# Kernel optimization log

Hardware: AMD Instinct MI355X
Metric: run time of the kernel (lower is better)

The kernel has to match this reference:

```python
import jax, jax.numpy as jnp
import numpy as np

EPS = 1e-6

def rms_norm(x, w):
    xf = x.astype(jnp.float32)
    xf = xf * jax.lax.rsqrt(jnp.mean(jnp.square(xf), axis=-1, keepdims=True) + EPS)
    return xf.astype(x.dtype) * w

def rotate_pairs(x):
    x = x.reshape(*x.shape[:-1], -1, 2)
    x1, x2 = x[..., 0], x[..., 1]
    return jnp.stack((-x2, x1), axis=-1).reshape(*x.shape[:-2], -1)

def apply_rope_axis(x, coords, inv_freq):
    # x: [B, H, T, axis_width]; coords: [T]; inv_freq: [axis_dim]
    angles = coords[:, None].astype(jnp.float32) * inv_freq[None, :]  # [T, axis_dim]
    cos = jnp.repeat(jnp.cos(angles), 2, axis=-1).astype(x.dtype)  # [T, axis_width]
    sin = jnp.repeat(jnp.sin(angles), 2, axis=-1).astype(x.dtype)
    return x * cos[None, None] + rotate_pairs(x) * sin[None, None]

def modulate(x, shift, scale):
    return x * (1.0 + scale[:, None, :]) + shift[:, None, :]

def setup_inputs() -> dict:
    key = jax.random.key(0)
    ks = jax.random.split(key, 16)
    B, T, D = 2, 2048, 1024
    HD = 64            # head_dim
    HID = 4096         # swiglu hidden (dim * mlp_ratio)
    CD = 1024          # cond_dim
    s = lambda n: 1.0 / np.sqrt(n)
    return {
        "x": jax.random.normal(ks[0], (B, T, D), jnp.float32),
        "cond": jax.random.normal(ks[1], (B, CD), jnp.float32),
        "norm1_w": jnp.ones((D,), jnp.float32),
        "qkv_w": jax.random.normal(ks[2], (3 * D, D), jnp.float32) * s(D),
        "q_norm_w": jnp.ones((HD,), jnp.float32),
        "k_norm_w": jnp.ones((HD,), jnp.float32),
        "proj_w": jax.random.normal(ks[3], (D, D), jnp.float32) * s(D),
        "proj_b": jnp.zeros((D,), jnp.float32),
        "norm2_w": jnp.ones((D,), jnp.float32),
        "fc1_w": jax.random.normal(ks[4], (2 * HID, D), jnp.float32) * s(D),
        "fc1_b": jnp.zeros((2 * HID,), jnp.float32),
        "fc2_w": jax.random.normal(ks[5], (D, HID), jnp.float32) * s(HID),
        "fc2_b": jnp.zeros((D,), jnp.float32),
        "ada_w": jax.random.normal(ks[6], (6 * D, CD), jnp.float32) * 0.02,
        "ada_b": jnp.zeros((6 * D,), jnp.float32),
        "height": 64,
        "width": 32,
    }

def reference(x, cond, norm1_w, qkv_w, q_norm_w, k_norm_w, proj_w, proj_b,
              norm2_w, fc1_w, fc1_b, fc2_w, fc2_b, ada_w, ada_b, height, width):
    B, T, D = x.shape
    HD = q_norm_w.shape[0]
    NH = D // HD
    scale = HD ** -0.5
    axis_dim = HD // 4
    axis_w = axis_dim * 2
    inv_freq = 1.0 / (10000.0 ** (jnp.arange(axis_dim, dtype=jnp.float32) / axis_dim))

    # AdaLN-Zero conditioning
    ada = jax.nn.silu(cond) @ ada_w.T + ada_b  # [B, 6D]
    sh_a, sc_a, g_a, sh_m, sc_m, g_m = jnp.split(ada, 6, axis=-1)

    # --- attention branch ---
    residual = x
    h = modulate(rms_norm(x, norm1_w), sh_a, sc_a)
    qkv = (h @ qkv_w.T).reshape(B, T, 3, NH, HD)
    q, k, v = qkv[:, :, 0], qkv[:, :, 1], qkv[:, :, 2]  # [B, T, NH, HD]
    q = rms_norm(q, q_norm_w)
    k = rms_norm(k, k_norm_w)
    q = q.transpose(0, 2, 1, 3)  # [B, NH, T, HD]
    k = k.transpose(0, 2, 1, 3)
    v = v.transpose(0, 2, 1, 3)

    # 2D RoPE: y coords on first axis_w dims, x coords on next axis_w dims
    yy, xx = jnp.meshgrid(jnp.arange(height), jnp.arange(width), indexing="ij")
    yy, xx = yy.reshape(-1), xx.reshape(-1)  # [T]
    q = jnp.concatenate([
        apply_rope_axis(q[..., :axis_w], yy, inv_freq),
        apply_rope_axis(q[..., axis_w:2 * axis_w], xx, inv_freq),
        q[..., 2 * axis_w:]], axis=-1)
    k = jnp.concatenate([
        apply_rope_axis(k[..., :axis_w], yy, inv_freq),
        apply_rope_axis(k[..., axis_w:2 * axis_w], xx, inv_freq),
        k[..., 2 * axis_w:]], axis=-1)

    attn = jax.nn.softmax(jnp.einsum("bhqd,bhkd->bhqk", q, k) * scale, axis=-1)
    h = jnp.einsum("bhqk,bhkd->bhqd", attn, v).transpose(0, 2, 1, 3).reshape(B, T, D)
    h = h @ proj_w.T + proj_b
    x = residual + g_a[:, None, :] * h

    # --- SwiGLU MLP branch ---
    residual = x
    h = modulate(rms_norm(x, norm2_w), sh_m, sc_m)
    value, gate = jnp.split(h @ fc1_w.T + fc1_b, 2, axis=-1)
    h = (value * jax.nn.silu(gate)) @ fc2_w.T + fc2_b
    return residual + g_m[:, None, :] * h
```

## Files before the change

### kernel.cpp

```cpp
#include <hip/hip_runtime.h>
#include <hip/hip_bf16.h>

#define B_   2
#define T_   2048
#define D_   1024
#define NH_  16
#define HD_  64
#define HID_ 4096
#define CD_  1024
#define SIX_D (6*D_)

typedef __bf16 bf16x8 __attribute__((ext_vector_type(8)));
typedef float  f32x4  __attribute__((ext_vector_type(4)));
typedef float  f32x16 __attribute__((ext_vector_type(16)));

__device__ __forceinline__ unsigned short f2bf(float f){
  union { float f; unsigned u; } v; v.f = f;
  unsigned r = v.u + 0x7FFFu + ((v.u >> 16) & 1u);
  return (unsigned short)(r >> 16);
}
__device__ __forceinline__ float bf2f(unsigned short u){
  union { unsigned x; float f; } v; v.x = ((unsigned)u) << 16; return v.f;
}

__device__ __forceinline__ void gl_lds16(const void* g, void* l){
  __builtin_amdgcn_global_load_lds(
      (__attribute__((address_space(1))) void*)const_cast<void*>(g),
      (__attribute__((address_space(3))) void*)l, 16, 0, 0);
}

__global__ void k_conv_all(const float* __restrict__ s0, const float* __restrict__ s1,
                           const float* __restrict__ s2, const float* __restrict__ s3,
                           unsigned short* __restrict__ d0, unsigned short* __restrict__ d1,
                           unsigned short* __restrict__ d2, unsigned short* __restrict__ d3){
  int bid = blockIdx.x;
  const float* s; unsigned short* d; int base;
  if (bid < 3072)      { s = s0; d = d0; base = bid; }
  else if (bid < 4096) { s = s1; d = d1; base = bid - 3072; }
  else if (bid < 12288){ s = s2; d = d2; base = bid - 4096; }
  else                 { s = s3; d = d3; base = bid - 12288; }
  int i = base*256 + threadIdx.x;
  float4 v = reinterpret_cast<const float4*>(s)[i];
  ushort4 o;
  o.x = f2bf(v.x); o.y = f2bf(v.y); o.z = f2bf(v.z); o.w = f2bf(v.w);
  reinterpret_cast<ushort4*>(d)[i] = o;
}

__global__ void k_ada(const float* __restrict__ cond, const float* __restrict__ ada_w,
                      const float* __restrict__ ada_b, float* __restrict__ ada){
  __shared__ float sc[CD_];
  int b = blockIdx.y;
  int tid = threadIdx.x;
  for (int i = tid; i < CD_; i += 256){
    float c = cond[b*CD_ + i];
    sc[i] = c / (1.f + __expf(-c));
  }
  __syncthreads();
  int col = blockIdx.x*256 + tid;
  const float* wr = ada_w + (size_t)col*CD_;
  float acc = 0.f;
  #pragma unroll 4
  for (int k = 0; k < CD_; k++) acc += sc[k]*wr[k];
  ada[b*SIX_D + col] = acc + ada_b[col];
}

__global__ void k_norm_mod(const float* __restrict__ x, const float* __restrict__ w,
                           const float* __restrict__ ada, int sh_off, int sc_off,
                           unsigned short* __restrict__ out){
  int row = blockIdx.x;
  int b = row >> 11;
  int tid = threadIdx.x;
  float4 xv = reinterpret_cast<const float4*>(x + (size_t)row*D_)[tid];
  float ss = xv.x*xv.x + xv.y*xv.y + xv.z*xv.z + xv.w*xv.w;
  #pragma unroll
  for (int m = 32; m > 0; m >>= 1) ss += __shfl_xor(ss, m, 64);
  __shared__ float red[4];
  int wave = tid >> 6;
  if ((tid & 63) == 0) red[wave] = ss;
  __syncthreads();
  float tot = red[0]+red[1]+red[2]+red[3];
  float rn = rsqrtf(tot * (1.f/(float)D_) + 1e-6f);
  float4 wv  = reinterpret_cast<const float4*>(w)[tid];
  float4 scv = reinterpret_cast<const float4*>(ada + b*SIX_D + sc_off)[tid];
  float4 shv = reinterpret_cast<const float4*>(ada + b*SIX_D + sh_off)[tid];
  ushort4 o;
  o.x = f2bf(xv.x*rn*wv.x*(1.f+scv.x)+shv.x);
  o.y = f2bf(xv.y*rn*wv.y*(1.f+scv.y)+shv.y);
  o.z = f2bf(xv.z*rn*wv.z*(1.f+scv.z)+shv.z);
  o.w = f2bf(xv.w*rn*wv.w*(1.f+scv.w)+shv.w);
  reinterpret_cast<ushort4*>(out + (size_t)row*D_)[tid] = o;
}

enum { EPI_F32 = 0, EPI_RESID = 1, EPI_BF16 = 2 };

template<int EPI>
__launch_bounds__(256)
__global__ void k_gemm_bt(const unsigned short* __restrict__ A,
                          const unsigned short* __restrict__ W,
                          int M, int N, int K,
                          void* __restrict__ outp,
                          const float* __restrict__ resid,
                          const float* __restrict__ ada, int g_off,
                          const float* __restrict__ bias){
  __shared__ __align__(16) unsigned short As[2][128*32];
  __shared__ __align__(16) unsigned short Bs[2][128*32];
  const int tid = threadIdx.x;
  const int wave = tid >> 6, lane = tid & 63;
  const int wm = (wave >> 1)*64, wn = (wave & 1)*64;
  const int m0 = blockIdx.y*128, n0 = blockIdx.x*128;
  const int fr = lane & 15, fq = lane >> 4;
  const int sl = (fq ^ ((fr >> 1) & 3))*8;
  f32x4 acc[4][4] = {};
  auto stage = [&](int buf, int k0){
    #pragma unroll
    for (int rr = 0; rr < 2; rr++){
      int idx = rr*256 + tid;
      int row = idx >> 2, c = idx & 3;
      int g = c ^ ((row >> 1) & 3);
      gl_lds16(A + (size_t)(m0 + row)*K + k0 + g*8, &As[buf][(idx & ~63)*8]);
      gl_lds16(W + (size_t)(n0 + row)*K + k0 + g*8, &Bs[buf][(idx & ~63)*8]);
    }
  };
  stage(0, 0);
  __syncthreads();
  const int NK = K >> 5;
  for (int t = 0; t < NK; t++){
    const int cur = t & 1;
    if (t + 1 < NK) stage(cur ^ 1, (t + 1)*32);
    bf16x8 af[4], bfr[4];
    #pragma unroll
    for (int i = 0; i < 4; i++){
      af[i]  = *(const bf16x8*)&As[cur][(wm + i*16 + fr)*32 + sl];
      bfr[i] = *(const bf16x8*)&Bs[cur][(wn + i*16 + fr)*32 + sl];
    }
    __builtin_amdgcn_s_setprio(1);
    #pragma unroll
    for (int i = 0; i < 4; i++)
      #pragma unroll
      for (int j = 0; j < 4; j++)
        acc[i][j] = __builtin_amdgcn_mfma_f32_16x16x32_bf16(af[i], bfr[j], acc[i][j], 0,0,0);
    __builtin_amdgcn_s_setprio(0);
    __syncthreads();
  }
  #pragma unroll
  for (int i = 0; i < 4; i++){
    #pragma unroll
    for (int j = 0; j < 4; j++){
      int col = n0 + wn + j*16 + fr;
      #pragma unroll
      for (int r = 0; r < 4; r++){
        int row = m0 + wm + i*16 + fq*4 + r;
        float v = acc[i][j][r];
        if (EPI == EPI_F32){
          ((float*)outp)[(size_t)row*N + col] = v;
        } else if (EPI == EPI_BF16){
          ((unsigned short*)outp)[(size_t)row*N + col] = f2bf(v);
        } else {
          int b = row >> 11;
          float g = ada[b*SIX_D + g_off + col];
          ((float*)outp)[(size_t)row*N + col] = resid[(size_t)row*N + col] + g*(v + bias[col]);
        }
      }
    }
  }
}

template<int EPI>
__launch_bounds__(256)
__global__ void k_gemm_bt64(const unsigned short* __restrict__ A,
                            const unsigned short* __restrict__ W,
                            int M, int N, int K,
                            void* __restrict__ outp,
                            const float* __restrict__ resid,
                            const float* __restrict__ ada, int g_off,
                            const float* __restrict__ bias){
  __shared__ __align__(16) unsigned short As[2][64*32];
  __shared__ __align__(16) unsigned short Bs[2][128*32];
  const int tid = threadIdx.x;
  const int wave = tid >> 6, lane = tid & 63;
  const int wm = (wave >> 1)*32, wn = (wave & 1)*64;
  const int m0 = blockIdx.y*64, n0 = blockIdx.x*128;
  const int fr = lane & 15, fq = lane >> 4;
  const int sl = (fq ^ ((fr >> 1) & 3))*8;
  f32x4 acc[2][4] = {};
  auto stage = [&](int buf, int k0){
    {
      int row = tid >> 2, c = tid & 3;
      int g = c ^ ((row >> 1) & 3);
      gl_lds16(A + (size_t)(m0 + row)*K + k0 + g*8, &As[buf][(tid & ~63)*8]);
    }
    #pragma unroll
    for (int rr = 0; rr < 2; rr++){
      int idx = rr*256 + tid;
      int row = idx >> 2, c = idx & 3;
      int g = c ^ ((row >> 1) & 3);
      gl_lds16(W + (size_t)(n0 + row)*K + k0 + g*8, &Bs[buf][(idx & ~63)*8]);
    }
  };
  stage(0, 0);
  __syncthreads();
  const int NK = K >> 5;
  for (int t = 0; t < NK; t++){
    const int cur = t & 1;
    if (t + 1 < NK) stage(cur ^ 1, (t + 1)*32);
    bf16x8 af[2], bfr[4];
    #pragma unroll
    for (int i = 0; i < 2; i++)
      af[i]  = *(const bf16x8*)&As[cur][(wm + i*16 + fr)*32 + sl];
    #pragma unroll
    for (int j = 0; j < 4; j++)
      bfr[j] = *(const bf16x8*)&Bs[cur][(wn + j*16 + fr)*32 + sl];
    __builtin_amdgcn_s_setprio(1);
    #pragma unroll
    for (int i = 0; i < 2; i++)
      #pragma unroll
      for (int j = 0; j < 4; j++)
        acc[i][j] = __builtin_amdgcn_mfma_f32_16x16x32_bf16(af[i], bfr[j], acc[i][j], 0,0,0);
    __builtin_amdgcn_s_setprio(0);
    __syncthreads();
  }
  #pragma unroll
  for (int i = 0; i < 2; i++){
    #pragma unroll
    for (int j = 0; j < 4; j++){
      int col = n0 + wn + j*16 + fr;
      #pragma unroll
      for (int r = 0; r < 4; r++){
        int row = m0 + wm + i*16 + fq*4 + r;
        float v = acc[i][j][r];
        if (EPI == EPI_F32){
          ((float*)outp)[(size_t)row*N + col] = v;
        } else if (EPI == EPI_BF16){
          ((unsigned short*)outp)[(size_t)row*N + col] = f2bf(v);
        } else {
          int b = row >> 11;
          float g = ada[b*SIX_D + g_off + col];
          ((float*)outp)[(size_t)row*N + col] = resid[(size_t)row*N + col] + g*(v + bias[col]);
        }
      }
    }
  }
}

__launch_bounds__(256)
__global__ void k_gemm_fc1(const unsigned short* __restrict__ A,
                           const unsigned short* __restrict__ W,
                           const float* __restrict__ bias,
                           unsigned short* __restrict__ out){
  __shared__ __align__(16) unsigned short As[2][128*32];
  __shared__ __align__(16) unsigned short Bv[2][64*32];
  __shared__ __align__(16) unsigned short Bg[2][64*32];
  const int K = D_;
  const int tid = threadIdx.x;
  const int wave = tid >> 6, lane = tid & 63;
  const int wm = (wave >> 1)*64, wn = (wave & 1)*32;
  const int m0 = blockIdx.y*128, n0 = blockIdx.x*64;
  const int fr = lane & 15, fq = lane >> 4;
  const int sl = (fq ^ ((fr >> 1) & 3))*8;
  f32x4 accv[4][2] = {}, accg[4][2] = {};
  auto stage = [&](int buf, int k0){
    #pragma unroll
    for (int rr = 0; rr < 2; rr++){
      int idx = rr*256 + tid;
      int row = idx >> 2, c = idx & 3;
      int g = c ^ ((row >> 1) & 3);
      gl_lds16(A + (size_t)(m0 + row)*K + k0 + g*8, &As[buf][(idx & ~63)*8]);
    }
    {
      int row = tid >> 2, c = tid & 3;
      int g = c ^ ((row >> 1) & 3);
      gl_lds16(W + (size_t)(n0 + row)*K + k0 + g*8,        &Bv[buf][(tid & ~63)*8]);
      gl_lds16(W + (size_t)(HID_ + n0 + row)*K + k0 + g*8, &Bg[buf][(tid & ~63)*8]);
    }
  };
  stage(0, 0);
  __syncthreads();
  const int NK = K >> 5;
  for (int t = 0; t < NK; t++){
    const int cur = t & 1;
    if (t + 1 < NK) stage(cur ^ 1, (t + 1)*32);
    bf16x8 af[4], bv[2], bg[2];
    #pragma unroll
    for (int i = 0; i < 4; i++)
      af[i] = *(const bf16x8*)&As[cur][(wm + i*16 + fr)*32 + sl];
    #pragma unroll
    for (int j = 0; j < 2; j++){
      bv[j] = *(const bf16x8*)&Bv[cur][(wn + j*16 + fr)*32 + sl];
      bg[j] = *(const bf16x8*)&Bg[cur][(wn + j*16 + fr)*32 + sl];
    }
    __builtin_amdgcn_s_setprio(1);
    #pragma unroll
    for (int i = 0; i < 4; i++)
      #pragma unroll
      for (int j = 0; j < 2; j++){
        accv[i][j] = __builtin_amdgcn_mfma_f32_16x16x32_bf16(af[i], bv[j], accv[i][j], 0,0,0);
        accg[i][j] = __builtin_amdgcn_mfma_f32_16x16x32_bf16(af[i], bg[j], accg[i][j], 0,0,0);
      }
    __builtin_amdgcn_s_setprio(0);
    __syncthreads();
  }
  #pragma unroll
  for (int i = 0; i < 4; i++){
    #pragma unroll
    for (int j = 0; j < 2; j++){
      int col = n0 + wn + j*16 + fr;
      #pragma unroll
      for (int r = 0; r < 4; r++){
        int row = m0 + wm + i*16 + fq*4 + r;
        float vv = accv[i][j][r] + bias[col];
        float gg = accg[i][j][r] + bias[HID_ + col];
        float h = vv * (gg / (1.f + __expf(-gg)));
        out[(size_t)row*HID_ + col] = f2bf(h);
      }
    }
  }
}

__global__ void k_qkv_post(const unsigned short* __restrict__ qkv,
                           const float* __restrict__ qw, const float* __restrict__ kw,
                           const int* __restrict__ wptr,
                           unsigned short* __restrict__ q, unsigned short* __restrict__ k){
  int idx = blockIdx.x*4 + (threadIdx.x >> 6);
  int h = idx & (NH_-1);
  int t = (idx >> 4) & (T_-1);
  int b = idx >> 15;
  int d = threadIdx.x & 63;
  const unsigned short* base = qkv + (size_t)(b*T_ + t)*3072;
  float qv = bf2f(base[h*64 + d]);
  float kv = bf2f(base[1024 + h*64 + d]);
  float sq = qv*qv, sk = kv*kv;
  #pragma unroll
  for (int m = 32; m > 0; m >>= 1){ sq += __shfl_xor(sq, m, 64); sk += __shfl_xor(sk, m, 64); }
  qv *= rsqrtf(sq*(1.f/64.f) + 1e-6f) * qw[d];
  kv *= rsqrtf(sk*(1.f/64.f) + 1e-6f) * kw[d];
  int width = wptr[0];
  int yy = t / width, xx = t - yy*width;
  int coord = (d < 32) ? yy : xx;
  int fi = (d & 31) >> 1;
  float ifreq = __expf(-(float)fi * (9.210340371976184f/16.f));
  float ang = (float)coord * ifreq;
  float cs = cosf(ang), sn = sinf(ang);
  float pq = __shfl_xor(qv, 1, 64);
  float pk = __shfl_xor(kv, 1, 64);
  float rq = (d & 1) ? pq : -pq;
  float rk = (d & 1) ? pk : -pk;
  qv = qv*cs + rq*sn;
  kv = kv*cs + rk*sn;
  size_t o = ((size_t)(b*NH_ + h)*T_ + t)*64 + d;
  q[o] = f2bf(qv); k[o] = f2bf(kv);
}

__global__ void k_vtrans(const unsigned short* __restrict__ qkv, unsigned short* __restrict__ vt){
  __shared__ __align__(16) unsigned short TT[64*64];
  int bh = blockIdx.y, t0 = blockIdx.x*64;
  int b = bh >> 4, h = bh & 15;
  int tid = threadIdx.x;
  #pragma unroll
  for (int it = 0; it < 2; it++){
    int i2 = it*256 + tid;
    int t = i2 >> 3, c8 = (i2 & 7)*8;
    union { uint4 v; unsigned short u[8]; } ld;
    ld.v = *(const uint4*)(qkv + (size_t)(b*T_ + t0 + t)*3072 + 2048 + h*64 + c8);
    #pragma unroll
    for (int e = 0; e < 8; e++){
      int c = c8 + e;
      int gp = (t >> 3) ^ ((c >> 2) & 7);
      TT[c*64 + gp*8 + (t & 7)] = ld.u[e];
    }
  }
  __syncthreads();
  #pragma unroll
  for (int it = 0; it < 2; it++){
    int i2 = it*256 + tid;
    int d = i2 >> 3, g = i2 & 7;
    int gp = g ^ ((d >> 2) & 7);
    *(uint4*)(vt + ((size_t)(bh*64 + d)*T_ + t0 + g*8)) = *(const uint4*)&TT[d*64 + gp*8];
  }
}

__launch_bounds__(128, 2)
__global__ void k_attn(const unsigned short* __restrict__ q,
                       const unsigned short* __restrict__ k,
                       const unsigned short* __restrict__ vt,
                       unsigned short* __restrict__ out){
  __shared__ __align__(16) unsigned short Kl[2][64*64];
  __shared__ __align__(16) unsigned short Vl[2][64*64];
  const int tid  = threadIdx.x;
  const int wave = tid >> 6;
  const int lane = tid & 63;
  const int ln   = lane & 31;
  const int hi   = lane >> 5;
  const int id = blockIdx.x;
  const int bh = id & 31;
  const int q0 = (id >> 5)*64 + wave*32;

  bf16x8 qf[4];
  {
    const unsigned short* qp = q + ((size_t)bh*T_ + q0 + ln)*HD_ + hi*8;
    #pragma unroll
    for (int kk = 0; kk < 4; kk++)
      qf[kk] = *(const bf16x8*)(qp + kk*16);
  }
  const unsigned short* kg = k  + (size_t)bh*T_*HD_;
  const unsigned short* vg = vt + (size_t)bh*HD_*T_;

  auto stage = [&](int buf, int kt){
    #pragma unroll
    for (int rr = 0; rr < 4; rr++){
      int idx = rr*128 + tid;
      int row = idx >> 3, c = idx & 7;
      int g = c ^ (row & 7);
      gl_lds16(kg + (size_t)(kt + row)*HD_ + g*8, &Kl[buf][(idx & ~63)*8]);
      gl_lds16(vg + (size_t)row*T_ + kt + g*8,    &Vl[buf][(idx & ~63)*8]);
    }
  };

  f32x16 o0 = {}, o1 = {};
  float ls[4] = {};
  const int vr0 = ln*64, vr1 = (32 + ln)*64;
  const int sw = ln & 7;

  stage(0, 0);
  __syncthreads();

  for (int t = 0; t < T_/64; t++){
    const int cur = t & 1, nxt = cur ^ 1;
    if (t + 1 < T_/64) stage(nxt, (t + 1)*64);
    const unsigned short* Kc = Kl[cur];
    const unsigned short* Vc = Vl[cur];
    #pragma unroll
    for (int s2 = 0; s2 < 2; s2++){
      bf16x8 kf[4];
      const int kb = (s2*32 + ln)*64;
      #pragma unroll
      for (int kk = 0; kk < 4; kk++){
        int ch = (kk*2 + hi) ^ sw;
        kf[kk] = *(const bf16x8*)&Kc[kb + ch*8];
      }
      f32x16 sa = {}, sb = {};
      __builtin_amdgcn_s_setprio(1);
      sa = __builtin_amdgcn_mfma_f32_32x32x16_bf16(kf[0], qf[0], sa, 0, 0, 0);
      sb = __builtin_amdgcn_mfma_f32_32x32x16_bf16(kf[1], qf[1], sb, 0, 0, 0);
      sa = __builtin_amdgcn_mfma_f32_32x32x16_bf16(kf[2], qf[2], sa, 0, 0, 0);
      sb = __builtin_amdgcn_mfma_f32_32x32x16_bf16(kf[3], qf[3], sb, 0, 0, 0);
      __builtin_amdgcn_s_setprio(0);
      union { uint2 u2[2]; bf16x8 v; } v0f[2], v1f[2];
      #pragma unroll
      for (int c = 0; c < 2; c++){
        int chA = (s2*4 + c*2)     ^ sw;
        int chB = (s2*4 + c*2 + 1) ^ sw;
        v0f[c].u2[0] = *(const uint2*)&Vc[vr0 + chA*8 + hi*4];
        v0f[c].u2[1] = *(const uint2*)&Vc[vr0 + chB*8 + hi*4];
        v1f[c].u2[0] = *(const uint2*)&Vc[vr1 + chA*8 + hi*4];
        v1f[c].u2[1] = *(const uint2*)&Vc[vr1 + chB*8 + hi*4];
      }
      f32x16 sv = sa + sb;
      float p[16];
      #pragma unroll
      for (int r = 0; r < 16; r++)
        p[r] = __expf(fminf(sv[r]*0.125f, 30.f));
      union { __bf16 h[16]; bf16x8 v[2]; } pa;
      #pragma unroll
      for (int r = 0; r < 16; r++){
        pa.h[r] = (__bf16)p[r];
        ls[r & 3] += p[r];
      }
      __builtin_amdgcn_s_setprio(1);
      o0 = __builtin_amdgcn_mfma_f32_32x32x16_bf16(pa.v[0], v0f[0].v, o0, 0, 0, 0);
      o1 = __builtin_amdgcn_mfma_f32_32x32x16_bf16(pa.v[0], v1f[0].v, o1, 0, 0, 0);
      o0 = __builtin_amdgcn_mfma_f32_32x32x16_bf16(pa.v[1], v0f[1].v, o0, 0, 0, 0);
      o1 = __builtin_amdgcn_mfma_f32_32x32x16_bf16(pa.v[1], v1f[1].v, o1, 0, 0, 0);
      __builtin_amdgcn_s_setprio(0);
    }
    __syncthreads();
  }

  float lsum = ls[0] + ls[1] + ls[2] + ls[3];
  lsum += __shfl_xor(lsum, 32, 64);
  float inv = 1.f / lsum;
  const int b = bh >> 4, h = bh & 15;
  unsigned short* ob = out + ((size_t)(b*T_ + q0))*D_ + h*64 + ln;
  #pragma unroll
  for (int r = 0; r < 16; r++){
    int qr = (r & 3) + 8*(r >> 2) + 4*hi;
    float invr = __shfl(inv, qr, 64);
    unsigned short* op = ob + (size_t)qr*D_;
    op[0]  = f2bf(o0[r]*invr);
    op[32] = f2bf(o1[r]*invr);
  }
}

extern "C" void kernel_launch(void* const* d_in, const int* in_sizes, int n_in,
                              void* d_out, int out_size, void* d_ws, size_t ws_size,
                              hipStream_t stream){
  const float* x      = (const float*)d_in[0];
  const float* cond   = (const float*)d_in[1];
  const float* norm1w = (const float*)d_in[2];
  const float* qkv_w  = (const float*)d_in[3];
  const float* q_nw   = (const float*)d_in[4];
  const float* k_nw   = (const float*)d_in[5];
  const float* proj_w = (const float*)d_in[6];
  const float* proj_b = (const float*)d_in[7];
  const float* norm2w = (const float*)d_in[8];
  const float* fc1_w  = (const float*)d_in[9];
  const float* fc1_b  = (const float*)d_in[10];
  const float* fc2_w  = (const float*)d_in[11];
  const float* fc2_b  = (const float*)d_in[12];
  const float* ada_w  = (const float*)d_in[13];
  const float* ada_b  = (const float*)d_in[14];
  const int*   wptr   = (const int*)d_in[16];
  float* out = (float*)d_out;

  char* ws = (char*)d_ws;
  size_t off = 0;
  auto alloc = [&](size_t bytes)->void*{
    void* p = ws + off; off += (bytes + 255) & ~(size_t)255; return p;
  };
  unsigned short* w_qkv  = (unsigned short*)alloc(3072ull*1024*2);
  unsigned short* w_proj = (unsigned short*)alloc(1024ull*1024*2);
  unsigned short* w_fc1  = (unsigned short*)alloc(8192ull*1024*2);
  unsigned short* w_fc2  = (unsigned short*)alloc(1024ull*4096*2);
  float* ada             = (float*)alloc((size_t)B_*SIX_D*4);
  unsigned short* h1     = (unsigned short*)alloc(4096ull*1024*2);
  char* R                = (char*)alloc(4096ull*3072*4);
  unsigned short* qkv_out= (unsigned short*)R;
  unsigned short* attn_o = (unsigned short*)R;
  float* x1              = (float*)(R + (size_t)B_*T_*D_*2);
  unsigned short* qb     = (unsigned short*)alloc(32ull*2048*64*2);
  unsigned short* kb     = (unsigned short*)alloc(32ull*2048*64*2);
  unsigned short* vt     = (unsigned short*)alloc(32ull*64*2048*2);
  unsigned short* mlp    = (unsigned short*)alloc(4096ull*4096*2);
  (void)ws_size; (void)in_sizes; (void)n_in; (void)out_size;

  k_conv_all<<<16384, 256, 0, stream>>>(qkv_w, proj_w, fc1_w, fc2_w, w_qkv, w_proj, w_fc1, w_fc2);

  k_ada<<<dim3(SIX_D/256, B_), 256, 0, stream>>>(cond, ada_w, ada_b, ada);
  k_norm_mod<<<B_*T_, 256, 0, stream>>>(x, norm1w, ada, 0, D_, h1);
  k_gemm_bt<EPI_BF16><<<dim3(3072/128, 4096/128), 256, 0, stream>>>(
      h1, w_qkv, B_*T_, 3*D_, D_, qkv_out, nullptr, nullptr, 0, nullptr);
  k_qkv_post<<<B_*T_*NH_/4, 256, 0, stream>>>(qkv_out, q_nw, k_nw, wptr, qb, kb);
  k_vtrans<<<dim3(T_/64, 32), 256, 0, stream>>>(qkv_out, vt);
  k_attn<<<1024, 128, 0, stream>>>(qb, kb, vt, attn_o);
  k_gemm_bt64<EPI_RESID><<<dim3(1024/128, 4096/64), 256, 0, stream>>>(
      attn_o, w_proj, B_*T_, D_, D_, x1, x, ada, 2*D_, proj_b);
  k_norm_mod<<<B_*T_, 256, 0, stream>>>(x1, norm2w, ada, 3*D_, 4*D_, h1);
  k_gemm_fc1<<<dim3(HID_/64, 4096/128), 256, 0, stream>>>(h1, w_fc1, fc1_b, mlp);
  k_gemm_bt64<EPI_RESID><<<dim3(1024/128, 4096/64), 256, 0, stream>>>(
      mlp, w_fc2, B_*T_, D_, HID_, out, x1, ada, 5*D_, fc2_b);
}
```

Before: 509.9 us.

## Pipeline GEMM LDS staging with fine-grained vmcnt waits and split ada reduction

All three GEMM kernels now precompute their global load pointers and advance them by 32 each step. They prefetch two K-tiles up front and wait with s_waitcnt vmcnt(N) plus s_barrier instead of a full __syncthreads drain, then issue the next stage load only after the compute barrier. The intent is to keep one tile of global-to-LDS loads in flight while the MFMAs run and to cut address arithmetic. Separately, k_ada splits its K dimension across four waves with a shared-memory reduction, launching four times as many blocks so the weight streaming is better parallelised. The hand-written vmcnt counts assume a fixed number of outstanding loads per stage, which is fragile if the compiler emits other vector memory ops.

Result: faster. 472.7 us (-7.3%).

```diff
diff --git a/kernel.cpp b/kernel.cpp
--- a/kernel.cpp
+++ b/kernel.cpp
@@ -49,6 +49,7 @@
 __global__ void k_ada(const float* __restrict__ cond, const float* __restrict__ ada_w,
                       const float* __restrict__ ada_b, float* __restrict__ ada){
   __shared__ float sc[CD_];
+  __shared__ float part[4][64];
   int b = blockIdx.y;
   int tid = threadIdx.x;
   for (int i = tid; i < CD_; i += 256){
@@ -56,12 +57,20 @@
     sc[i] = c / (1.f + __expf(-c));
   }
   __syncthreads();
-  int col = blockIdx.x*256 + tid;
-  const float* wr = ada_w + (size_t)col*CD_;
+  int col = blockIdx.x*64 + (tid & 63);
+  int qk  = tid >> 6;
+  const float* wr = ada_w + (size_t)col*CD_ + qk*256;
+  const float* scq = sc + qk*256;
   float acc = 0.f;
   #pragma unroll 4
-  for (int k = 0; k < CD_; k++) acc += sc[k]*wr[k];
-  ada[b*SIX_D + col] = acc + ada_b[col];
+  for (int k = 0; k < 256; k++) acc += scq[k]*wr[k];
+  part[qk][tid & 63] = acc;
+  __syncthreads();
+  if (tid < 64){
+    float a = part[0][tid] + part[1][tid] + part[2][tid] + part[3][tid];
+    int c = blockIdx.x*64 + tid;
+    ada[b*SIX_D + c] = a + ada_b[c];
+  }
 }
 
 __global__ void k_norm_mod(const float* __restrict__ x, const float* __restrict__ w,
@@ -110,23 +119,30 @@
   const int m0 = blockIdx.y*128, n0 = blockIdx.x*128;
   const int fr = lane & 15, fq = lane >> 4;
   const int sl = (fq ^ ((fr >> 1) & 3))*8;
+  const int r0 = tid >> 2, c0 = tid & 3;
+  const int g0 = c0 ^ ((r0 >> 1) & 3);
+  const int r1 = r0 + 64;
+  const int g1 = c0 ^ ((r1 >> 1) & 3);
+  const unsigned short* gA0 = A + (size_t)(m0 + r0)*K + g0*8;
+  const unsigned short* gA1 = A + (size_t)(m0 + r1)*K + g1*8;
+  const unsigned short* gB0 = W + (size_t)(n0 + r0)*K + g0*8;
+  const unsigned short* gB1 = W + (size_t)(n0 + r1)*K + g1*8;
+  const int l0 = (tid & ~63)*8, l1 = ((256 + tid) & ~63)*8;
   f32x4 acc[4][4] = {};
-  auto stage = [&](int buf, int k0){
-    #pragma unroll
-    for (int rr = 0; rr < 2; rr++){
-      int idx = rr*256 + tid;
-      int row = idx >> 2, c = idx & 3;
-      int g = c ^ ((row >> 1) & 3);
-      gl_lds16(A + (size_t)(m0 + row)*K + k0 + g*8, &As[buf][(idx & ~63)*8]);
-      gl_lds16(W + (size_t)(n0 + row)*K + k0 + g*8, &Bs[buf][(idx & ~63)*8]);
-    }
+  auto stage = [&](int buf){
+    gl_lds16(gA0, &As[buf][l0]);
+    gl_lds16(gA1, &As[buf][l1]);
+    gl_lds16(gB0, &Bs[buf][l0]);
+    gl_lds16(gB1, &Bs[buf][l1]);
+    gA0 += 32; gA1 += 32; gB0 += 32; gB1 += 32;
   };
-  stage(0, 0);
-  __syncthreads();
+  stage(0); stage(1);
   const int NK = K >> 5;
   for (int t = 0; t < NK; t++){
     const int cur = t & 1;
-    if (t + 1 < NK) stage(cur ^ 1, (t + 1)*32);
+    if (t < NK - 1) asm volatile("s_waitcnt vmcnt(4)" ::: "memory");
+    else            asm volatile("s_waitcnt vmcnt(0)" ::: "memory");
+    __builtin_amdgcn_s_barrier();
     bf16x8 af[4], bfr[4];
     #pragma unroll
     for (int i = 0; i < 4; i++){
@@ -140,7 +156,8 @@
       for (int j = 0; j < 4; j++)
         acc[i][j] = __builtin_amdgcn_mfma_f32_16x16x32_bf16(af[i], bfr[j], acc[i][j], 0,0,0);
     __builtin_amdgcn_s_setprio(0);
-    __syncthreads();
+    __builtin_amdgcn_s_barrier();
+    if (t + 2 < NK) stage(cur);
   }
   #pragma unroll
   for (int i = 0; i < 4; i++){
@@ -182,27 +199,28 @@
   const int m0 = blockIdx.y*64, n0 = blockIdx.x*128;
   const int fr = lane & 15, fq = lane >> 4;
   const int sl = (fq ^ ((fr >> 1) & 3))*8;
+  const int r0 = tid >> 2, c0 = tid & 3;
+  const int g0 = c0 ^ ((r0 >> 1) & 3);
+  const int r1 = r0 + 64;
+  const int g1 = c0 ^ ((r1 >> 1) & 3);
+  const unsigned short* gA0 = A + (size_t)(m0 + r0)*K + g0*8;
+  const unsigned short* gB0 = W + (size_t)(n0 + r0)*K + g0*8;
+  const unsigned short* gB1 = W + (size_t)(n0 + r1)*K + g1*8;
+  const int l0 = (tid & ~63)*8, l1 = ((256 + tid) & ~63)*8;
   f32x4 acc[2][4] = {};
-  auto stage = [&](int buf, int k0){
-    {
-      int row = tid >> 2, c = tid & 3;
-      int g = c ^ ((row >> 1) & 3);
-      gl_lds16(A + (size_t)(m0 + row)*K + k0 + g*8, &As[buf][(tid & ~63)*8]);
-    }
-    #pragma unroll
-    for (int rr = 0; rr < 2; rr++){
-      int idx = rr*256 + tid;
-      int row = idx >> 2, c = idx & 3;
-      int g = c ^ ((row >> 1) & 3);
-      gl_lds16(W + (size_t)(n0 + row)*K + k0 + g*8, &Bs[buf][(idx & ~63)*8]);
-    }
+  auto stage = [&](int buf){
+    gl_lds16(gA0, &As[buf][l0]);
+    gl_lds16(gB0, &Bs[buf][l0]);
+    gl_lds16(gB1, &Bs[buf][l1]);
+    gA0 += 32; gB0 += 32; gB1 += 32;
   };
-  stage(0, 0);
-  __syncthreads();
+  stage(0); stage(1);
   const int NK = K >> 5;
   for (int t = 0; t < NK; t++){
     const int cur = t & 1;
-    if (t + 1 < NK) stage(cur ^ 1, (t + 1)*32);
+    if (t < NK - 1) asm volatile("s_waitcnt vmcnt(3)" ::: "memory");
+    else            asm volatile("s_waitcnt vmcnt(0)" ::: "memory");
+    __builtin_amdgcn_s_barrier();
     bf16x8 af[2], bfr[4];
     #pragma unroll
     for (int i = 0; i < 2; i++)
@@ -217,7 +235,8 @@
       for (int j = 0; j < 4; j++)
         acc[i][j] = __builtin_amdgcn_mfma_f32_16x16x32_bf16(af[i], bfr[j], acc[i][j], 0,0,0);
     __builtin_amdgcn_s_setprio(0);
-    __syncthreads();
+    __builtin_amdgcn_s_barrier();
+    if (t + 2 < NK) stage(cur);
   }
   #pragma unroll
   for (int i = 0; i < 2; i++){
@@ -257,28 +276,30 @@
   const int m0 = blockIdx.y*128, n0 = blockIdx.x*64;
   const int fr = lane & 15, fq = lane >> 4;
   const int sl = (fq ^ ((fr >> 1) & 3))*8;
+  const int r0 = tid >> 2, c0 = tid & 3;
+  const int g0 = c0 ^ ((r0 >> 1) & 3);
+  const int r1 = r0 + 64;
+  const int g1 = c0 ^ ((r1 >> 1) & 3);
+  const unsigned short* gA0 = A + (size_t)(m0 + r0)*K + g0*8;
+  const unsigned short* gA1 = A + (size_t)(m0 + r1)*K + g1*8;
+  const unsigned short* gBv = W + (size_t)(n0 + r0)*K + g0*8;
+  const unsigned short* gBg = W + (size_t)(HID_ + n0 + r0)*K + g0*8;
+  const int l0 = (tid & ~63)*8, l1 = ((256 + tid) & ~63)*8;
   f32x4 accv[4][2] = {}, accg[4][2] = {};
-  auto stage = [&](int buf, int k0){
-    #pragma unroll
-    for (int rr = 0; rr < 2; rr++){
-      int idx = rr*256 + tid;
-      int row = idx >> 2, c = idx & 3;
-      int g = c ^ ((row >> 1) & 3);
-      gl_lds16(A + (size_t)(m0 + row)*K + k0 + g*8, &As[buf][(idx & ~63)*8]);
-    }
-    {
-      int row = tid >> 2, c = tid & 3;
-      int g = c ^ ((row >> 1) & 3);
-      gl_lds16(W + (size_t)(n0 + row)*K + k0 + g*8,        &Bv[buf][(tid & ~63)*8]);
-      gl_lds16(W + (size_t)(HID_ + n0 + row)*K + k0 + g*8, &Bg[buf][(tid & ~63)*8]);
-    }
+  auto stage = [&](int buf){
+    gl_lds16(gA0, &As[buf][l0]);
+    gl_lds16(gA1, &As[buf][l1]);
+    gl_lds16(gBv, &Bv[buf][l0]);
+    gl_lds16(gBg, &Bg[buf][l0]);
+    gA0 += 32; gA1 += 32; gBv += 32; gBg += 32;
   };
-  stage(0, 0);
-  __syncthreads();
+  stage(0); stage(1);
   const int NK = K >> 5;
   for (int t = 0; t < NK; t++){
     const int cur = t & 1;
-    if (t + 1 < NK) stage(cur ^ 1, (t + 1)*32);
+    if (t < NK - 1) asm volatile("s_waitcnt vmcnt(4)" ::: "memory");
+    else            asm volatile("s_waitcnt vmcnt(0)" ::: "memory");
+    __builtin_amdgcn_s_barrier();
     bf16x8 af[4], bv[2], bg[2];
     #pragma unroll
     for (int i = 0; i < 4; i++)
@@ -297,7 +318,8 @@
         accg[i][j] = __builtin_amdgcn_mfma_f32_16x16x32_bf16(af[i], bg[j], accg[i][j], 0,0,0);
       }
     __builtin_amdgcn_s_setprio(0);
-    __syncthreads();
+    __builtin_amdgcn_s_barrier();
+    if (t + 2 < NK) stage(cur);
   }
   #pragma unroll
   for (int i = 0; i < 4; i++){
@@ -534,7 +556,7 @@
 
   k_conv_all<<<16384, 256, 0, stream>>>(qkv_w, proj_w, fc1_w, fc2_w, w_qkv, w_proj, w_fc1, w_fc2);
 
-  k_ada<<<dim3(SIX_D/256, B_), 256, 0, stream>>>(cond, ada_w, ada_b, ada);
+  k_ada<<<dim3(SIX_D/64, B_), 256, 0, stream>>>(cond, ada_w, ada_b, ada);
   k_norm_mod<<<B_*T_, 256, 0, stream>>>(x, norm1w, ada, 0, D_, h1);
   k_gemm_bt<EPI_BF16><<<dim3(3072/128, 4096/128), 256, 0, stream>>>(
       h1, w_qkv, B_*T_, 3*D_, D_, qkv_out, nullptr, nullptr, 0, nullptr);
```
